# Performance work log

Measured on AMD Instinct MI355X. Metric: run time of the kernel, lower is better.

The kernel has to match this reference:

```python
import jax, jax.numpy as jnp
import numpy as np

NUM_CATS = 5
EPS = 1e-6


def setup_inputs() -> dict:
    key = jax.random.key(0)
    k1, k2, k3, k4 = jax.random.split(key, 4)
    B, C, H, W = 64, 3, 256, 256
    restored = jax.random.normal(k1, (B, C, H, W), dtype=jnp.float32)
    clean_patch_1 = jax.random.normal(k2, (B, C, H, W), dtype=jnp.float32)
    un = jax.random.uniform(k3, (B, C, H, W), dtype=jnp.float32)
    de_id = jax.random.randint(k4, (B,), 0, NUM_CATS)
    return {"restored": restored, "clean_patch_1": clean_patch_1,
            "de_id": de_id, "un": un}


def _loss(restored, clean, un, de_id):
    B, C, H, W = restored.shape
    E = C * H * W  # elements per sample
    dt = restored.dtype

    onehot = (de_id[:, None] == jnp.arange(NUM_CATS)[None, :])  # [B,5] bool
    m = onehot.astype(dt)                                        # [B,5]
    counts = onehot.sum(0)                                       # [5] int
    nonempty = counts > 0
    safe_counts = jnp.maximum(counts, 1).astype(dt)              # avoid 0-div

    # Per-category mean uncertainty map: un_map[c] = mean_{i: de_id[i]=c} un[i] + eps
    un_sum = jnp.einsum('bk,bchw->kchw', m, un)                  # [5,C,H,W]
    un_map = un_sum / safe_counts[:, None, None, None] + EPS     # [5,C,H,W]
    s = 1.0 / un_map                                             # [5,C,H,W]

    # Per-sample scaled L1 (s gathered by each sample's category)
    absdiff = jnp.abs(clean - restored)                          # [B,C,H,W]
    scaled_sum_per_sample = (absdiff * s[de_id]).sum(axis=(1, 2, 3))  # [B]
    abs_sum_per_sample = absdiff.sum(axis=(1, 2, 3))                  # [B]

    cat_scaled_sum = jnp.einsum('bk,b->k', m, scaled_sum_per_sample)  # [5]
    cat_abs_sum = jnp.einsum('bk,b->k', m, abs_sum_per_sample)        # [5]

    # NOTE: the original code never clears un_hq_list/un_lq_list between
    # categories, so the L1 at category c is the mean over ALL samples from
    # categories 0..c (each scaled by its OWN category's s). Replicate that
    # via cumulative sums/counts over the category axis.
    cum_scaled = jnp.cumsum(cat_scaled_sum)                      # [5]
    cum_elems = jnp.cumsum(counts).astype(dt) * E                # [5]
    cum_l1 = cum_scaled / jnp.maximum(cum_elems, 1.0)            # [5]

    old_loss = jnp.where(nonempty, cat_abs_sum / (safe_counts * E), 0.0)
    un_num = un_map.mean(axis=(1, 2, 3))                         # [5]
    bn = jnp.where(nonempty, 2.0 * jnp.log(un_num), 0.0)
    unc_l1 = jnp.where(nonempty, cum_l1, 0.0)

    cat_losses = unc_l1 + bn                                     # [5]
    num = nonempty.sum().astype(dt)
    total = cat_losses.sum() / num
    return total, cat_losses, old_loss, bn, unc_l1


def reference(restored, clean_patch_1, de_id, un):
    return _loss(restored, clean_patch_1, un, de_id)
```

## Files before the change

kernel.cpp:

```cpp
#include <hip/hip_runtime.h>
#include <math.h>

#define NCAT  5
#define BATCH 64
#define ELEMS 196608
#define EPSV  1e-6f

typedef float v4f __attribute__((ext_vector_type(4)));

#define WIN1   1024
#define NBLK1  (ELEMS / WIN1)
#define TPB1   1024
#define CHUNK1 16
#define GRP1   4

#define NSLAB  12
#define SLABSZ (ELEMS / NSLAB)
#define NBLK2  (BATCH * NSLAB)

#define WS_S   0
#define WS_P1  (NCAT * ELEMS)
#define WS_P2  (WS_P1 + NCAT * NBLK1)

static __device__ __forceinline__ v4f vfma(float m, v4f a, v4f b) {
    v4f r;
    r.x = fmaf(m, a.x, b.x);
    r.y = fmaf(m, a.y, b.y);
    r.z = fmaf(m, a.z, b.z);
    r.w = fmaf(m, a.w, b.w);
    return r;
}

__global__ __launch_bounds__(TPB1) void pass1_kernel(
    const float* __restrict__ un,
    const int*   __restrict__ de_id,
    float*       __restrict__ s_buf,
    float*       __restrict__ p1)
{
    __shared__ int   sh_de[BATCH];
    __shared__ float sh_inv[NCAT];
    __shared__ v4f   sbuf[2][4][NCAT][64];
    __shared__ float sh_part[4][NCAT];

    const int tid  = threadIdx.x;
    const int lane = tid & 63;
    const int wave = tid >> 6;
    const int ws   = wave & 3;
    const int bc   = wave >> 2;

    if (tid < BATCH) {
        int k = de_id[tid];
        sh_de[tid] = k;
        #pragma unroll
        for (int j = 0; j < NCAT; ++j) {
            unsigned long long m = __ballot(k == j);
            if (tid == j) {
                int c = __popcll(m);
                sh_inv[j] = 1.0f / (float)(c > 0 ? c : 1);
            }
        }
    }
    __syncthreads();

    const size_t STR4 = ELEMS / 4;
    const size_t pos4 = (size_t)blockIdx.x * (WIN1 / 4) + ws * 64 + lane;
    const v4f* up4 = (const v4f*)(un) + pos4;

    v4f acc[NCAT];
    #pragma unroll
    for (int j = 0; j < NCAT; ++j) acc[j] = (v4f)0.f;

    v4f ub[2][GRP1];
    #pragma unroll
    for (int i = 0; i < GRP1; ++i)
        ub[0][i] = up4[(size_t)(bc * CHUNK1 + i) * STR4];

    #pragma unroll
    for (int g = 0; g < CHUNK1 / GRP1; ++g) {
        const int cur = g & 1;
        const int nxt = cur ^ 1;
        if (g < CHUNK1 / GRP1 - 1) {
            #pragma unroll
            for (int i = 0; i < GRP1; ++i)
                ub[nxt][i] = up4[(size_t)(bc * CHUNK1 + (g + 1) * GRP1 + i) * STR4];
        }
        #pragma unroll
        for (int i = 0; i < GRP1; ++i) {
            const int k = sh_de[bc * CHUNK1 + g * GRP1 + i];
            #pragma unroll
            for (int j = 0; j < NCAT; ++j) {
                float m = (k == j) ? 1.0f : 0.0f;
                acc[j] = vfma(m, ub[cur][i], acc[j]);
            }
        }
    }

    if (bc >= 2) {
        #pragma unroll
        for (int j = 0; j < NCAT; ++j) sbuf[bc - 2][ws][j][lane] = acc[j];
    }
    __syncthreads();
    if (bc < 2) {
        #pragma unroll
        for (int j = 0; j < NCAT; ++j) acc[j] += sbuf[bc][ws][j][lane];
    }
    __syncthreads();
    if (bc == 1) {
        #pragma unroll
        for (int j = 0; j < NCAT; ++j) sbuf[0][ws][j][lane] = acc[j];
    }
    __syncthreads();
    if (bc == 0) {
        float vals[NCAT];
        #pragma unroll
        for (int j = 0; j < NCAT; ++j) {
            v4f a = acc[j] + sbuf[0][ws][j][lane];

            v4f um, sv;
            um.x = fmaf(a.x, sh_inv[j], EPSV);
            um.y = fmaf(a.y, sh_inv[j], EPSV);
            um.z = fmaf(a.z, sh_inv[j], EPSV);
            um.w = fmaf(a.w, sh_inv[j], EPSV);
            sv.x = 1.0f / um.x;
            sv.y = 1.0f / um.y;
            sv.z = 1.0f / um.z;
            sv.w = 1.0f / um.w;
            ((v4f*)s_buf)[(size_t)j * STR4 + pos4] = sv;

            vals[j] = (a.x + a.y) + (a.z + a.w);
        }
        #pragma unroll
        for (int j = 0; j < NCAT; ++j) {
            float v = vals[j];
            #pragma unroll
            for (int off = 32; off >= 1; off >>= 1)
                v += __shfl_down(v, off, 64);
            if (lane == 0) sh_part[ws][j] = v;
        }
    }
    __syncthreads();
    if (tid < NCAT)
        p1[tid * NBLK1 + blockIdx.x] =
            sh_part[0][tid] + sh_part[1][tid] + sh_part[2][tid] + sh_part[3][tid];
}

__global__ __launch_bounds__(256) void pass2_kernel(
    const float* __restrict__ restored,
    const float* __restrict__ clean,
    const int*   __restrict__ de_id,
    const float* __restrict__ s_buf,
    float*       __restrict__ p2)
{
    __shared__ float sred[4][2];

    const int tid  = threadIdx.x;
    const int lane = tid & 63;
    const int wave = tid >> 6;

    const int b   = blockIdx.x / NSLAB;
    const int sl  = blockIdx.x % NSLAB;
    const int cat = de_id[b];

    const size_t base4 = (size_t)sl * (SLABSZ / 4) + (size_t)wave * (SLABSZ / 16)
                       + (size_t)lane;
    const v4f* cp = (const v4f*)(clean)    + (size_t)b   * (ELEMS / 4) + base4;
    const v4f* rp = (const v4f*)(restored) + (size_t)b   * (ELEMS / 4) + base4;
    const v4f* sp = (const v4f*)(s_buf)    + (size_t)cat * (ELEMS / 4) + base4;

    float ssum = 0.f, asum = 0.f;
    #pragma unroll 16
    for (int it = 0; it < SLABSZ / 16 / 64; ++it) {
        v4f c  = __builtin_nontemporal_load(cp + it * 64);
        v4f r  = __builtin_nontemporal_load(rp + it * 64);
        v4f sv = sp[it * 64];
        float a0 = fabsf(c.x - r.x);
        float a1 = fabsf(c.y - r.y);
        float a2 = fabsf(c.z - r.z);
        float a3 = fabsf(c.w - r.w);
        asum += (a0 + a1) + (a2 + a3);
        ssum = fmaf(a0, sv.x, ssum);
        ssum = fmaf(a1, sv.y, ssum);
        ssum = fmaf(a2, sv.z, ssum);
        ssum = fmaf(a3, sv.w, ssum);
    }

    #pragma unroll
    for (int off = 32; off >= 1; off >>= 1) {
        ssum += __shfl_down(ssum, off, 64);
        asum += __shfl_down(asum, off, 64);
    }
    if (lane == 0) { sred[wave][0] = ssum; sred[wave][1] = asum; }
    __syncthreads();
    if (tid == 0) {
        float s = sred[0][0] + sred[1][0] + sred[2][0] + sred[3][0];
        float a = sred[0][1] + sred[1][1] + sred[2][1] + sred[3][1];
        p2[blockIdx.x]         = s;
        p2[NBLK2 + blockIdx.x] = a;
    }
}

__global__ __launch_bounds__(1024) void epilogue_kernel(
    const int*   __restrict__ de_id,
    const float* __restrict__ p1,
    const float* __restrict__ p2,
    float*       __restrict__ out)
{
    __shared__ int   sh_cnt[NCAT];
    __shared__ int   sh_cat[BATCH];
    __shared__ float sh_acc[3 * NCAT];

    const int tid  = threadIdx.x;
    const int lane = tid & 63;
    const int wave = tid >> 6;

    if (tid < BATCH) {
        int k = de_id[tid];
        sh_cat[tid] = k;
        #pragma unroll
        for (int j = 0; j < NCAT; ++j) {
            unsigned long long m = __ballot(k == j);
            if (tid == j) sh_cnt[j] = __popcll(m);
        }
    }
    __syncthreads();

    float v = 0.f;
    if (wave < 5) {
        for (int it = 0; it < NBLK2 / 64; ++it) {
            int col = it * 64 + lane;
            v += (sh_cat[col / NSLAB] == wave) ? p2[col] : 0.f;
        }
    } else if (wave < 10) {
        const int j = wave - 5;
        for (int it = 0; it < NBLK2 / 64; ++it) {
            int col = it * 64 + lane;
            v += (sh_cat[col / NSLAB] == j) ? p2[NBLK2 + col] : 0.f;
        }
    } else if (wave < 15) {
        const int j = wave - 10;
        for (int it = 0; it < NBLK1 / 64; ++it)
            v += p1[j * NBLK1 + it * 64 + lane];
    }
    #pragma unroll
    for (int off = 32; off >= 1; off >>= 1)
        v += __shfl_down(v, off, 64);
    if (lane == 0 && wave < 15) sh_acc[wave] = v;
    __syncthreads();

    if (tid == 0) {
        const float Ef = (float)ELEMS;
        float cum_s = 0.f;
        long  cum_c = 0;
        float total = 0.f;
        int   num   = 0;

        float cat_losses[NCAT], old_loss[NCAT], bn[NCAT], unc_l1[NCAT];

        for (int j = 0; j < NCAT; ++j) {
            cum_s += sh_acc[j];
            cum_c += sh_cnt[j];
            float cum_elems = (float)cum_c * Ef;
            float cum_l1    = cum_s / fmaxf(cum_elems, 1.0f);

            bool  ne   = sh_cnt[j] > 0;
            float safe = (float)(ne ? sh_cnt[j] : 1);

            old_loss[j]  = ne ? sh_acc[NCAT + j] / (safe * Ef) : 0.f;
            float un_num = sh_acc[2 * NCAT + j] / (safe * Ef) + EPSV;
            bn[j]        = ne ? 2.0f * logf(un_num) : 0.f;
            unc_l1[j]    = ne ? cum_l1 : 0.f;
            cat_losses[j] = unc_l1[j] + bn[j];
            total += cat_losses[j];
            num   += ne ? 1 : 0;
        }
        total /= (float)num;

        out[0] = total;
        for (int j = 0; j < NCAT; ++j) {
            out[1 + j]  = cat_losses[j];
            out[6 + j]  = old_loss[j];
            out[11 + j] = bn[j];
            out[16 + j] = unc_l1[j];
        }
    }
}

extern "C" void kernel_launch(void* const* d_in, const int* in_sizes, int n_in,
                              void* d_out, int out_size, void* d_ws, size_t ws_size,
                              hipStream_t stream) {
    (void)in_sizes; (void)n_in; (void)out_size; (void)ws_size;
    const float* restored = (const float*)d_in[0];
    const float* clean    = (const float*)d_in[1];
    const int*   de_id    = (const int*)d_in[2];
    const float* un       = (const float*)d_in[3];
    float* out   = (float*)d_out;
    float* ws    = (float*)d_ws;
    float* s_buf = ws + WS_S;
    float* p1    = ws + WS_P1;
    float* p2    = ws + WS_P2;

    pass1_kernel<<<NBLK1, TPB1, 0, stream>>>(un, de_id, s_buf, p1);
    pass2_kernel<<<NBLK2, 256, 0, stream>>>(restored, clean, de_id, s_buf, p2);
    epilogue_kernel<<<1, 1024, 0, stream>>>(de_id, p1, p2, out);
}
```

Measured before the change: 164.5 us.

## Restructure pass1 to per-category blocks gathering only matching samples

Pass1 now launches one block per (category, slab) and builds a compacted list of samples belonging to that category, summing only those rows of the uncertainty tensor. This removes the masked FMA over all five categories and the multi-stage shared-memory reduction of the previous design. Per-block work now depends on category sizes, and there is less memory-level parallelism per thread.

```diff
diff --git a/kernel.cpp b/kernel.cpp
--- a/kernel.cpp
+++ b/kernel.cpp
@@ -8,11 +8,10 @@
 
 typedef float v4f __attribute__((ext_vector_type(4)));
 
-#define WIN1   1024
-#define NBLK1  (ELEMS / WIN1)
-#define TPB1   1024
-#define CHUNK1 16
-#define GRP1   4
+#define NSLAB1 64
+#define SLAB1  (ELEMS / NSLAB1)
+#define NP1    NSLAB1
+#define NBLKP1 (NCAT * NSLAB1)
 
 #define NSLAB  12
 #define SLABSZ (ELEMS / NSLAB)
@@ -20,128 +19,92 @@
 
 #define WS_S   0
 #define WS_P1  (NCAT * ELEMS)
-#define WS_P2  (WS_P1 + NCAT * NBLK1)
-
-static __device__ __forceinline__ v4f vfma(float m, v4f a, v4f b) {
-    v4f r;
-    r.x = fmaf(m, a.x, b.x);
-    r.y = fmaf(m, a.y, b.y);
-    r.z = fmaf(m, a.z, b.z);
-    r.w = fmaf(m, a.w, b.w);
-    return r;
-}
-
-__global__ __launch_bounds__(TPB1) void pass1_kernel(
+#define WS_P2  (WS_P1 + NCAT * NP1)
+
+__global__ __launch_bounds__(256) void pass1_kernel(
     const float* __restrict__ un,
     const int*   __restrict__ de_id,
     float*       __restrict__ s_buf,
     float*       __restrict__ p1)
 {
-    __shared__ int   sh_de[BATCH];
-    __shared__ float sh_inv[NCAT];
-    __shared__ v4f   sbuf[2][4][NCAT][64];
-    __shared__ float sh_part[4][NCAT];
+    __shared__ int   sh_list[BATCH];
+    __shared__ int   sh_n;
+    __shared__ float sh_inv;
+    __shared__ float sred[4];
 
     const int tid  = threadIdx.x;
     const int lane = tid & 63;
     const int wave = tid >> 6;
-    const int ws   = wave & 3;
-    const int bc   = wave >> 2;
+
+    const int c  = blockIdx.x / NSLAB1;
+    const int sl = blockIdx.x % NSLAB1;
 
     if (tid < BATCH) {
-        int k = de_id[tid];
-        sh_de[tid] = k;
-        #pragma unroll
-        for (int j = 0; j < NCAT; ++j) {
-            unsigned long long m = __ballot(k == j);
-            if (tid == j) {
-                int c = __popcll(m);
-                sh_inv[j] = 1.0f / (float)(c > 0 ? c : 1);
-            }
-        }
-    }
-    __syncthreads();
+        bool match = (de_id[tid] == c);
+        unsigned long long mask = __ballot(match);
+        if (match)
+            sh_list[__popcll(mask & ((1ull << tid) - 1ull))] = tid;
+        if (tid == 0) {
+            int n = __popcll(mask);
+            sh_n   = n;
+            sh_inv = 1.0f / (float)(n > 0 ? n : 1);
+        }
+    }
+    __syncthreads();
+    const int   n   = sh_n;
+    const float inv = sh_inv;
 
     const size_t STR4 = ELEMS / 4;
-    const size_t pos4 = (size_t)blockIdx.x * (WIN1 / 4) + ws * 64 + lane;
-    const v4f* up4 = (const v4f*)(un) + pos4;
-
-    v4f acc[NCAT];
+    const size_t off4 = (size_t)sl * (SLAB1 / 4) + (size_t)wave * (SLAB1 / 16)
+                      + (size_t)lane;
+    const v4f* up = (const v4f*)(un) + off4;
+
+    v4f acc0 = (v4f)0.f, acc1 = (v4f)0.f, acc2 = (v4f)0.f;
+
+    v4f a0 = (v4f)0.f, a1 = (v4f)0.f, a2 = (v4f)0.f;
+    v4f b0 = (v4f)0.f, b1 = (v4f)0.f, b2 = (v4f)0.f;
+
+    if (n > 0) {
+        const size_t o = (size_t)sh_list[0] * STR4;
+        a0 = up[o]; a1 = up[o + 64]; a2 = up[o + 128];
+    }
+    for (int i = 0; i < n; i += 2) {
+        if (i + 1 < n) {
+            const size_t o = (size_t)sh_list[i + 1] * STR4;
+            b0 = up[o]; b1 = up[o + 64]; b2 = up[o + 128];
+        }
+        acc0 += a0; acc1 += a1; acc2 += a2;
+        if (i + 2 < n) {
+            const size_t o = (size_t)sh_list[i + 2] * STR4;
+            a0 = up[o]; a1 = up[o + 64]; a2 = up[o + 128];
+        }
+        if (i + 1 < n) { acc0 += b0; acc1 += b1; acc2 += b2; }
+    }
+
+    v4f* sp = (v4f*)(s_buf) + (size_t)c * STR4 + off4;
+    v4f um, sv;
+    um.x = fmaf(acc0.x, inv, EPSV); um.y = fmaf(acc0.y, inv, EPSV);
+    um.z = fmaf(acc0.z, inv, EPSV); um.w = fmaf(acc0.w, inv, EPSV);
+    sv.x = 1.0f/um.x; sv.y = 1.0f/um.y; sv.z = 1.0f/um.z; sv.w = 1.0f/um.w;
+    sp[0] = sv;
+    um.x = fmaf(acc1.x, inv, EPSV); um.y = fmaf(acc1.y, inv, EPSV);
+    um.z = fmaf(acc1.z, inv, EPSV); um.w = fmaf(acc1.w, inv, EPSV);
+    sv.x = 1.0f/um.x; sv.y = 1.0f/um.y; sv.z = 1.0f/um.z; sv.w = 1.0f/um.w;
+    sp[64] = sv;
+    um.x = fmaf(acc2.x, inv, EPSV); um.y = fmaf(acc2.y, inv, EPSV);
+    um.z = fmaf(acc2.z, inv, EPSV); um.w = fmaf(acc2.w, inv, EPSV);
+    sv.x = 1.0f/um.x; sv.y = 1.0f/um.y; sv.z = 1.0f/um.z; sv.w = 1.0f/um.w;
+    sp[128] = sv;
+
+    v4f t = acc0 + acc1 + acc2;
+    float v = (t.x + t.y) + (t.z + t.w);
     #pragma unroll
-    for (int j = 0; j < NCAT; ++j) acc[j] = (v4f)0.f;
-
-    v4f ub[2][GRP1];
-    #pragma unroll
-    for (int i = 0; i < GRP1; ++i)
-        ub[0][i] = up4[(size_t)(bc * CHUNK1 + i) * STR4];
-
-    #pragma unroll
-    for (int g = 0; g < CHUNK1 / GRP1; ++g) {
-        const int cur = g & 1;
-        const int nxt = cur ^ 1;
-        if (g < CHUNK1 / GRP1 - 1) {
-            #pragma unroll
-            for (int i = 0; i < GRP1; ++i)
-                ub[nxt][i] = up4[(size_t)(bc * CHUNK1 + (g + 1) * GRP1 + i) * STR4];
-        }
-        #pragma unroll
-        for (int i = 0; i < GRP1; ++i) {
-            const int k = sh_de[bc * CHUNK1 + g * GRP1 + i];
-            #pragma unroll
-            for (int j = 0; j < NCAT; ++j) {
-                float m = (k == j) ? 1.0f : 0.0f;
-                acc[j] = vfma(m, ub[cur][i], acc[j]);
-            }
-        }
-    }
-
-    if (bc >= 2) {
-        #pragma unroll
-        for (int j = 0; j < NCAT; ++j) sbuf[bc - 2][ws][j][lane] = acc[j];
-    }
-    __syncthreads();
-    if (bc < 2) {
-        #pragma unroll
-        for (int j = 0; j < NCAT; ++j) acc[j] += sbuf[bc][ws][j][lane];
-    }
-    __syncthreads();
-    if (bc == 1) {
-        #pragma unroll
-        for (int j = 0; j < NCAT; ++j) sbuf[0][ws][j][lane] = acc[j];
-    }
-    __syncthreads();
-    if (bc == 0) {
-        float vals[NCAT];
-        #pragma unroll
-        for (int j = 0; j < NCAT; ++j) {
-            v4f a = acc[j] + sbuf[0][ws][j][lane];
-
-            v4f um, sv;
-            um.x = fmaf(a.x, sh_inv[j], EPSV);
-            um.y = fmaf(a.y, sh_inv[j], EPSV);
-            um.z = fmaf(a.z, sh_inv[j], EPSV);
-            um.w = fmaf(a.w, sh_inv[j], EPSV);
-            sv.x = 1.0f / um.x;
-            sv.y = 1.0f / um.y;
-            sv.z = 1.0f / um.z;
-            sv.w = 1.0f / um.w;
-            ((v4f*)s_buf)[(size_t)j * STR4 + pos4] = sv;
-
-            vals[j] = (a.x + a.y) + (a.z + a.w);
-        }
-        #pragma unroll
-        for (int j = 0; j < NCAT; ++j) {
-            float v = vals[j];
-            #pragma unroll
-            for (int off = 32; off >= 1; off >>= 1)
-                v += __shfl_down(v, off, 64);
-            if (lane == 0) sh_part[ws][j] = v;
-        }
-    }
-    __syncthreads();
-    if (tid < NCAT)
-        p1[tid * NBLK1 + blockIdx.x] =
-            sh_part[0][tid] + sh_part[1][tid] + sh_part[2][tid] + sh_part[3][tid];
+    for (int off = 32; off >= 1; off >>= 1)
+        v += __shfl_down(v, off, 64);
+    if (lane == 0) sred[wave] = v;
+    __syncthreads();
+    if (tid == 0)
+        p1[c * NP1 + sl] = sred[0] + sred[1] + sred[2] + sred[3];
 }
 
 __global__ __launch_bounds__(256) void pass2_kernel(
@@ -238,8 +201,9 @@
         }
     } else if (wave < 15) {
         const int j = wave - 10;
-        for (int it = 0; it < NBLK1 / 64; ++it)
-            v += p1[j * NBLK1 + it * 64 + lane];
+        #pragma unroll
+        for (int it = 0; it < NP1 / 64; ++it)
+            v += p1[j * NP1 + it * 64 + lane];
     }
     #pragma unroll
     for (int off = 32; off >= 1; off >>= 1)
@@ -299,7 +263,7 @@
     float* p1    = ws + WS_P1;
     float* p2    = ws + WS_P2;
 
-    pass1_kernel<<<NBLK1, TPB1, 0, stream>>>(un, de_id, s_buf, p1);
+    pass1_kernel<<<NBLKP1, 256, 0, stream>>>(un, de_id, s_buf, p1);
     pass2_kernel<<<NBLK2, 256, 0, stream>>>(restored, clean, de_id, s_buf, p2);
     epilogue_kernel<<<1, 1024, 0, stream>>>(de_id, p1, p2, out);
 }
```

Result: no change. 162.6 us (-1.2%).
